# Performance work log

Measured on AMD Instinct MI355X. Metric: run time of the kernel, lower is better.

## Reference

```python
import jax, jax.numpy as jnp
import numpy as np

B, T, D = 2, 2048, 1024
H, DH = 16, 64          # num_heads, size_per_head
NU = H * DH             # num_units == 1024


def setup_inputs() -> dict:
    key = jax.random.key(0)
    ks = jax.random.split(key, 8)
    s = 0.02
    return {
        "queries": jax.random.normal(ks[0], (B, T, D), jnp.float32),
        "keys": jax.random.normal(ks[1], (B, T, D), jnp.float32),
        "Wq": jax.random.normal(ks[2], (D, NU), jnp.float32) * s,
        "bq": jnp.zeros((NU,), jnp.float32),
        "Wk": jax.random.normal(ks[3], (D, NU), jnp.float32) * s,
        "bk": jnp.zeros((NU,), jnp.float32),
        "Wv": jax.random.normal(ks[4], (D, NU), jnp.float32) * s,
        "bv": jnp.zeros((NU,), jnp.float32),
    }


def reference(queries, keys, Wq, bq, Wk, bk, Wv, bv):
    # QKV projections
    q = queries @ Wq + bq            # [B, T, NU]
    k = keys @ Wk + bk
    v = keys @ Wv + bv
    # split heads: [B, T, H, DH] -> [B, H, T, DH]
    q_ = q.reshape(B, T, H, DH).transpose(0, 2, 1, 3)
    k_ = k.reshape(B, T, H, DH).transpose(0, 2, 1, 3)
    v_ = v.reshape(B, T, H, DH).transpose(0, 2, 1, 3)
    # scores scaled by num_units**-0.5 (full hidden dim, as in source)
    scores = jnp.einsum("bhqd,bhkd->bhqk", q_, k_) * (NU ** -0.5)
    # causal mask: triu(ones).T == lower-triangular; zeros -> -inf
    causal = jnp.tril(jnp.ones((T, T), bool))
    scores = jnp.where(causal, scores, -jnp.inf)
    weights = jax.nn.softmax(scores, axis=-1)   # [B, H, T, T]
    # dropout is identity in eval/reference
    out = jnp.einsum("bhqk,bhkd->bhqd", weights, v_)  # [B, H, T, DH]
    # merge heads back to [B, T, NU]
    out = out.transpose(0, 2, 1, 3).reshape(B, T, NU)
    return out, weights
```

## Files before the change

kernel.cpp:

```cpp
#include <hip/hip_runtime.h>
#include <cstddef>
#include <cstdint>

namespace {
constexpr int B_ = 2, T_ = 2048, D_ = 1024, H_ = 16, DH_ = 64, NU_ = 1024;
constexpr float SCALE = 0.03125f;
constexpr size_t OUT_ELEMS = (size_t)B_ * T_ * NU_;
}

using f4  = __attribute__((ext_vector_type(4))) float;
using s8v = __attribute__((ext_vector_type(8))) short;
using s4v = __attribute__((ext_vector_type(4))) short;

#define MFMA16(a, b, c) __builtin_amdgcn_mfma_f32_16x16x32_bf16((a), (b), (c), 0, 0, 0)

__device__ __forceinline__ float4 ld4(const float* p) { return *reinterpret_cast<const float4*>(p); }
__device__ __forceinline__ void st4(float* p, const float4 v) { *reinterpret_cast<float4*>(p) = v; }
__device__ __forceinline__ short f2bf(float f) {
    union { float f; uint32_t u; } v{f};
    uint32_t r = (v.u + 0x7fffu + ((v.u >> 16) & 1u)) >> 16;
    return (short)r;
}

#if __has_builtin(__builtin_amdgcn_global_load_lds)
#define HAVE_GLOAD_LDS 1
__device__ __forceinline__ void load_lds16(const void* g, void* l) {
    __builtin_amdgcn_global_load_lds(
        (const __attribute__((address_space(1))) void*)g,
        (__attribute__((address_space(3))) void*)l, 16, 0, 0);
}
#else
#define HAVE_GLOAD_LDS 0
#endif

__global__ __launch_bounds__(256) void cvt_x_kernel(
    const float* __restrict__ q, const float* __restrict__ k,
    short* __restrict__ qx, short* __restrict__ kx)
{
    const float* src = blockIdx.y ? k : q;
    short* dst       = blockIdx.y ? kx : qx;
    size_t i = ((size_t)blockIdx.x * 256 + threadIdx.x) * 8;
    float4 a = ld4(src + i), b = ld4(src + i + 4);
    s8v o = { f2bf(a.x), f2bf(a.y), f2bf(a.z), f2bf(a.w),
              f2bf(b.x), f2bf(b.y), f2bf(b.z), f2bf(b.w) };
    *reinterpret_cast<s8v*>(dst + i) = o;
}

__global__ __launch_bounds__(256) void cvt_w_kernel(
    const float* __restrict__ Wq, const float* __restrict__ Wk,
    const float* __restrict__ Wv, short* __restrict__ wt3)
{
    const int z = blockIdx.z;
    const float* W = (z == 0) ? Wq : (z == 1) ? Wk : Wv;
    short* dst = wt3 + (size_t)z * D_ * NU_;
    const int n0 = blockIdx.x * 64, k0 = blockIdx.y * 64;
    __shared__ float tl[64][68];
    const int rr = threadIdx.x >> 2, cc = (threadIdx.x & 3) * 16;
    const float* s = W + (size_t)(k0 + rr) * NU_ + n0 + cc;
    st4(&tl[rr][cc + 0],  ld4(s + 0));
    st4(&tl[rr][cc + 4],  ld4(s + 4));
    st4(&tl[rr][cc + 8],  ld4(s + 8));
    st4(&tl[rr][cc + 12], ld4(s + 12));
    __syncthreads();
    short* d = dst + (size_t)(n0 + rr) * D_ + k0 + cc;
#pragma unroll
    for (int c = 0; c < 4; ++c) {
        s4v o = { f2bf(tl[cc + c * 4 + 0][rr]), f2bf(tl[cc + c * 4 + 1][rr]),
                  f2bf(tl[cc + c * 4 + 2][rr]), f2bf(tl[cc + c * 4 + 3][rr]) };
        *reinterpret_cast<s4v*>(d + c * 4) = o;
    }
}

__global__ __launch_bounds__(256) void proj_mfma(
    const short* __restrict__ qx, const short* __restrict__ kx,
    const short* __restrict__ wt3,
    const float* __restrict__ bq, const float* __restrict__ bk,
    const float* __restrict__ bv,
    short* __restrict__ qb, short* __restrict__ kb, short* __restrict__ vt)
{
    const int lin = blockIdx.z * 256 + blockIdx.y * 8 + blockIdx.x;
    const int virt = (lin & 7) * 96 + (lin >> 3);
    const int z = virt >> 8, rem = virt & 255;
    const int m0 = (rem >> 3) * 128, n0 = (rem & 7) * 128;

    const short* __restrict__ X  = (z == 0) ? qx : kx;
    const short* __restrict__ Wt = wt3 + (size_t)z * D_ * NU_;
    const float* __restrict__ bias = (z == 0) ? bq : (z == 1) ? bk : bv;

    const int t = threadIdx.x, w = t >> 6, l = t & 63;
    const int lr = l & 15, lg = l >> 4;
    const int wr = w >> 1, wc = w & 1;

    __shared__ short Asl[128 * 64];
    __shared__ short Bsl[128 * 64];

    f4 acc[4][4];
#pragma unroll
    for (int m = 0; m < 4; ++m)
#pragma unroll
        for (int n = 0; n < 4; ++n) acc[m][n] = (f4){0.f, 0.f, 0.f, 0.f};

    for (int k0 = 0; k0 < D_; k0 += 64) {
#if HAVE_GLOAD_LDS
#pragma unroll
        for (int j = 0; j < 4; ++j) {
            const int c0 = (w * 4 + j) * 64;
            const int c  = c0 + l;
            const int row = c >> 3, qo = (c & 7) * 8;
            load_lds16(X  + (size_t)(m0 + row) * D_ + k0 + qo, (char*)Asl + (size_t)c0 * 16);
            load_lds16(Wt + (size_t)(n0 + row) * D_ + k0 + qo, (char*)Bsl + (size_t)c0 * 16);
        }
        __syncthreads();
#else
        {
            const int sr = t >> 1, sc = (t & 1) * 32;
            s8v a0 = *reinterpret_cast<const s8v*>(X  + (size_t)(m0 + sr) * D_ + k0 + sc);
            s8v a1 = *reinterpret_cast<const s8v*>(X  + (size_t)(m0 + sr) * D_ + k0 + sc + 8);
            s8v a2 = *reinterpret_cast<const s8v*>(X  + (size_t)(m0 + sr) * D_ + k0 + sc + 16);
            s8v a3 = *reinterpret_cast<const s8v*>(X  + (size_t)(m0 + sr) * D_ + k0 + sc + 24);
            s8v b0 = *reinterpret_cast<const s8v*>(Wt + (size_t)(n0 + sr) * D_ + k0 + sc);
            s8v b1 = *reinterpret_cast<const s8v*>(Wt + (size_t)(n0 + sr) * D_ + k0 + sc + 8);
            s8v b2 = *reinterpret_cast<const s8v*>(Wt + (size_t)(n0 + sr) * D_ + k0 + sc + 16);
            s8v b3 = *reinterpret_cast<const s8v*>(Wt + (size_t)(n0 + sr) * D_ + k0 + sc + 24);
            __syncthreads();
            *reinterpret_cast<s8v*>(&Asl[sr * 64 + sc])      = a0;
            *reinterpret_cast<s8v*>(&Asl[sr * 64 + sc + 8])  = a1;
            *reinterpret_cast<s8v*>(&Asl[sr * 64 + sc + 16]) = a2;
            *reinterpret_cast<s8v*>(&Asl[sr * 64 + sc + 24]) = a3;
            *reinterpret_cast<s8v*>(&Bsl[sr * 64 + sc])      = b0;
            *reinterpret_cast<s8v*>(&Bsl[sr * 64 + sc + 8])  = b1;
            *reinterpret_cast<s8v*>(&Bsl[sr * 64 + sc + 16]) = b2;
            *reinterpret_cast<s8v*>(&Bsl[sr * 64 + sc + 24]) = b3;
            __syncthreads();
        }
#endif

#pragma unroll
        for (int kk = 0; kk < 2; ++kk) {
            s8v af[4], bf[4];
#pragma unroll
            for (int m = 0; m < 4; ++m)
                af[m] = *reinterpret_cast<const s8v*>(
                    &Asl[(wr * 64 + m * 16 + lr) * 64 + kk * 32 + lg * 8]);
#pragma unroll
            for (int n = 0; n < 4; ++n)
                bf[n] = *reinterpret_cast<const s8v*>(
                    &Bsl[(wc * 64 + n * 16 + lr) * 64 + kk * 32 + lg * 8]);
#pragma unroll
            for (int m = 0; m < 4; ++m)
#pragma unroll
                for (int n = 0; n < 4; ++n)
                    acc[m][n] = MFMA16(af[m], bf[n], acc[m][n]);
        }
        __syncthreads();
    }

    if (z < 2) {
        short* __restrict__ Y = (z == 0) ? qb : kb;
#pragma unroll
        for (int n = 0; n < 4; ++n) {
            const int col = n0 + wc * 64 + n * 16 + lr;
            const float bval = bias[col];
#pragma unroll
            for (int m = 0; m < 4; ++m) {
                const int row0 = m0 + wr * 64 + m * 16 + lg * 4;
#pragma unroll
                for (int r = 0; r < 4; ++r)
                    Y[(size_t)(row0 + r) * NU_ + col] = f2bf(acc[m][n][r] + bval);
            }
        }
    } else {
#pragma unroll
        for (int n = 0; n < 4; ++n) {
            const int col = n0 + wc * 64 + n * 16 + lr;
            const float bval = bias[col];
            const int hh = col >> 6, dd = col & 63;
#pragma unroll
            for (int m = 0; m < 4; ++m) {
                const int Mi = m0 + wr * 64 + m * 16 + lg * 4;
                const int bb = Mi >> 11, t0 = Mi & 2047;
                s4v o = { f2bf(acc[m][n][0] + bval), f2bf(acc[m][n][1] + bval),
                          f2bf(acc[m][n][2] + bval), f2bf(acc[m][n][3] + bval) };
                *reinterpret_cast<s4v*>(vt + ((size_t)(bb * 16 + hh) * 64 + dd) * T_ + t0) = o;
            }
        }
    }
}

__global__ __launch_bounds__(256) void attn_pv_mfma(
    const short* __restrict__ qb, const short* __restrict__ kb,
    const short* __restrict__ vt, float* __restrict__ rsws,
    float* __restrict__ out)
{
    const int lin = blockIdx.x;
    const int xcd = lin & 7, v = lin >> 3;
    const int bh  = xcd * 4 + (v >> 6);
    const int g32 = 63 - (v & 63);
    const int b = bh >> 4, h = bh & 15;
    const int r0 = g32 * 32;
    const int t = threadIdx.x, w = t >> 6, l = t & 63;
    const int lr = l & 15, lg = l >> 4;
    const int tile16 = (r0 + 31) >> 6;
    const int rlocA  = r0 - tile16 * 64 + lr;

    __shared__ __align__(16) char smem[16 * 1024 + 512];
    short* Pl    = (short*)smem;
    float* OA    = (float*)smem;
    float* rsbuf = (float*)(smem + 16 * 1024);

    const short* qrowA = qb + (size_t)(b * T_ + r0 + lr) * NU_ + h * DH_ + lg * 8;
    const s8v qA0 = *reinterpret_cast<const s8v*>(qrowA);
    const s8v qA1 = *reinterpret_cast<const s8v*>(qrowA + 32);
    const s8v qB0 = *reinterpret_cast<const s8v*>(qrowA + 16 * NU_);
    const s8v qB1 = *reinterpret_cast<const s8v*>(qrowA + 16 * NU_ + 32);

    f4 accA[4], accB[4];
#pragma unroll
    for (int nt = 0; nt < 4; ++nt) {
        accA[nt] = (f4){0.f, 0.f, 0.f, 0.f};
        accB[nt] = (f4){0.f, 0.f, 0.f, 0.f};
    }
    float rsumA = 0.f, rsumB = 0.f;
    const f4 zf = (f4){0.f, 0.f, 0.f, 0.f};
    const int sw = (lr & 7) << 3;
    const short* kbase0 = kb + (size_t)(b * T_) * NU_ + h * DH_ + lg * 8;
    short* const PlA = &Pl[w * 1024 + lr * 64];
    short* const PlB = &Pl[4096 + w * 1024 + lr * 64];

    for (int ch = w; ch <= tile16; ch += 4) {
        const int jc = ch * 64;
        const bool diag = (ch == tile16);
        const short* kbase = kbase0 + (size_t)jc * NU_;

#pragma unroll
        for (int nt = 0; nt < 4; ++nt) {
            const short* kr = kbase + (size_t)(nt * 16 + lr) * NU_;
            s8v kf0 = *reinterpret_cast<const s8v*>(kr);
            s8v kf1 = *reinterpret_cast<const s8v*>(kr + 32);
            f4 aA = MFMA16(kf0, qA0, zf);
            f4 sA = MFMA16(kf1, qA1, aA);
            f4 aB = MFMA16(kf0, qB0, zf);
            f4 sB = MFMA16(kf1, qB1, aB);

            const int jl = nt * 16 + lg * 4;
            float eA[4], eB[4];
#pragma unroll
            for (int r = 0; r < 4; ++r) {
                float vA = __expf(sA[r] * SCALE);
                float vB = __expf(sB[r] * SCALE);
                if (diag && (jl + r > rlocA))      vA = 0.f;
                if (diag && (jl + r > rlocA + 16)) vB = 0.f;
                eA[r] = vA; eB[r] = vB;
            }
            rsumA += (eA[0] + eA[1]) + (eA[2] + eA[3]);
            rsumB += (eB[0] + eB[1]) + (eB[2] + eB[3]);
            const int colp = jl ^ sw;
            s4v pA = { f2bf(eA[0]), f2bf(eA[1]), f2bf(eA[2]), f2bf(eA[3]) };
            s4v pB = { f2bf(eB[0]), f2bf(eB[1]), f2bf(eB[2]), f2bf(eB[3]) };
            *reinterpret_cast<s4v*>(PlA + colp) = pA;
            *reinterpret_cast<s4v*>(PlB + colp) = pB;
        }

        s8v pfA0 = *reinterpret_cast<const s8v*>(PlA + ((lg * 8) ^ sw));
        s8v pfA1 = *reinterpret_cast<const s8v*>(PlA + ((32 + lg * 8) ^ sw));
        s8v pfB0 = *reinterpret_cast<const s8v*>(PlB + ((lg * 8) ^ sw));
        s8v pfB1 = *reinterpret_cast<const s8v*>(PlB + ((32 + lg * 8) ^ sw));
#pragma unroll
        for (int nt = 0; nt < 4; ++nt) {
            const short* vr = vt + (size_t)(bh * 64 + nt * 16 + lr) * T_ + jc + lg * 8;
            s8v vf0 = *reinterpret_cast<const s8v*>(vr);
            s8v vf1 = *reinterpret_cast<const s8v*>(vr + 32);
            accA[nt] = MFMA16(pfA0, vf0, accA[nt]);
            accA[nt] = MFMA16(pfA1, vf1, accA[nt]);
            accB[nt] = MFMA16(pfB0, vf0, accB[nt]);
            accB[nt] = MFMA16(pfB1, vf1, accB[nt]);
        }
    }

    rsumA += __shfl_xor(rsumA, 16); rsumA += __shfl_xor(rsumA, 32);
    rsumB += __shfl_xor(rsumB, 16); rsumB += __shfl_xor(rsumB, 32);

    __syncthreads();
    if (lg == 0) {
        rsbuf[w * 16 + lr]      = rsumA;
        rsbuf[64 + w * 16 + lr] = rsumB;
    }

#pragma unroll
    for (int nt = 0; nt < 4; ++nt)
        st4(&OA[(size_t)(w * 64 + l) * 16 + nt * 4], *(const float4*)&accA[nt]);
    __syncthreads();
    {
        float osum[4] = {0.f, 0.f, 0.f, 0.f};
#pragma unroll
        for (int wv = 0; wv < 4; ++wv) {
            float4 p = *(const float4*)&OA[(size_t)(wv * 64 + l) * 16 + w * 4];
#pragma unroll
            for (int r = 0; r < 4; ++r) osum[r] += (&p.x)[r];
        }
#pragma unroll
        for (int r = 0; r < 4; ++r) {
            const int ro = lg * 4 + r;
            const float rt = rsbuf[ro] + rsbuf[16 + ro] + rsbuf[32 + ro] + rsbuf[48 + ro];
            out[(size_t)(b * T_ + r0 + ro) * NU_ + h * DH_ + w * 16 + lr] = osum[r] / rt;
        }
        if (w == 0 && t < 16) {
            rsws[(size_t)bh * T_ + r0 + t] =
                rsbuf[t] + rsbuf[16 + t] + rsbuf[32 + t] + rsbuf[48 + t];
            rsws[(size_t)bh * T_ + r0 + 16 + t] =
                rsbuf[64 + t] + rsbuf[80 + t] + rsbuf[96 + t] + rsbuf[112 + t];
        }
    }
    __syncthreads();

#pragma unroll
    for (int nt = 0; nt < 4; ++nt)
        st4(&OA[(size_t)(w * 64 + l) * 16 + nt * 4], *(const float4*)&accB[nt]);
    __syncthreads();
    {
        float osum[4] = {0.f, 0.f, 0.f, 0.f};
#pragma unroll
        for (int wv = 0; wv < 4; ++wv) {
            float4 p = *(const float4*)&OA[(size_t)(wv * 64 + l) * 16 + w * 4];
#pragma unroll
            for (int r = 0; r < 4; ++r) osum[r] += (&p.x)[r];
        }
#pragma unroll
        for (int r = 0; r < 4; ++r) {
            const int ro = lg * 4 + r;
            const float rt = rsbuf[64 + ro] + rsbuf[80 + ro] + rsbuf[96 + ro] + rsbuf[112 + ro];
            out[(size_t)(b * T_ + r0 + 16 + ro) * NU_ + h * DH_ + w * 16 + lr] = osum[r] / rt;
        }
    }
}

__global__ __launch_bounds__(256) void attn_wts_mfma(
    const short* __restrict__ qb, const short* __restrict__ kb,
    const float* __restrict__ rsws, float* __restrict__ wts)
{
    const int lin = blockIdx.x;
    const int xcd = lin & 7, v = lin >> 3;
    const int bh  = xcd * 4 + (v >> 7);
    const int rem = v & 127;
    const int qt2 = 15 - (rem >> 3);
    const int jb  = rem & 7;
    const int b = bh >> 4, h = bh & 15;
    const int r0 = qt2 * 128;
    const int chmax = 2 * qt2 + 1;
    const int t = threadIdx.x, w = t >> 6, l = t & 63;
    const int lr = l & 15, lg = l >> 4;

    const int iA = r0 + w * 16 + lr;
    const int iB = iA + 64;

    const short* qrowA = qb + (size_t)(b * T_ + iA) * NU_ + h * DH_ + lg * 8;
    const s8v qA0 = *reinterpret_cast<const s8v*>(qrowA);
    const s8v qA1 = *reinterpret_cast<const s8v*>(qrowA + 32);
    const s8v qB0 = *reinterpret_cast<const s8v*>(qrowA + 64 * NU_);
    const s8v qB1 = *reinterpret_cast<const s8v*>(qrowA + 64 * NU_ + 32);
    const f4 zf = (f4){0.f, 0.f, 0.f, 0.f};

    const float invA = 1.f / rsws[(size_t)bh * T_ + iA];
    const float invB = 1.f / rsws[(size_t)bh * T_ + iB];
    float* const wrowA = &wts[((size_t)bh * T_ + iA) * T_];
    float* const wrowB = &wts[((size_t)bh * T_ + iB) * T_];
    const short* kbase0 = kb + (size_t)(b * T_) * NU_ + h * DH_ + lg * 8;

#pragma unroll
    for (int cx = 0; cx < 4; ++cx) {
        const int ch = jb * 4 + cx;
        const int jc = ch * 64;
        if (ch <= chmax) {
            const short* kbase = kbase0 + (size_t)jc * NU_;
            f4 sA[4], sB[4];
#pragma unroll
            for (int nt = 0; nt < 4; ++nt) {
                const short* kr = kbase + (size_t)(nt * 16 + lr) * NU_;
                s8v kf0 = *reinterpret_cast<const s8v*>(kr);
                s8v kf1 = *reinterpret_cast<const s8v*>(kr + 32);
                f4 aA = MFMA16(kf0, qA0, zf);
                sA[nt] = MFMA16(kf1, qA1, aA);
                f4 aB = MFMA16(kf0, qB0, zf);
                sB[nt] = MFMA16(kf1, qB1, aB);
            }
#pragma unroll
            for (int nt = 0; nt < 4; ++nt) {
                float4 oA, oB;
                float* eA = &oA.x;
                float* eB = &oB.x;
#pragma unroll
                for (int r = 0; r < 4; ++r) {
                    const int j = jc + nt * 16 + lg * 4 + r;
                    eA[r] = (j <= iA) ? __expf(sA[nt][r] * SCALE) * invA : 0.f;
                    eB[r] = (j <= iB) ? __expf(sB[nt][r] * SCALE) * invB : 0.f;
                }
                st4(wrowA + jc + nt * 16 + lg * 4, oA);
                st4(wrowB + jc + nt * 16 + lg * 4, oB);
            }
        } else {
            const float4 z4 = make_float4(0.f, 0.f, 0.f, 0.f);
#pragma unroll
            for (int half = 0; half < 2; ++half) {
                float* dst = &wts[((size_t)bh * T_ + r0 + half * 64 + (t >> 2)) * T_
                                  + jc + (t & 3) * 16];
                st4(dst + 0, z4); st4(dst + 4, z4);
                st4(dst + 8, z4); st4(dst + 12, z4);
            }
        }
    }
}

extern "C" void kernel_launch(void* const* d_in, const int* in_sizes, int n_in,
                              void* d_out, int out_size, void* d_ws, size_t ws_size,
                              hipStream_t stream)
{
    const float* queries = (const float*)d_in[0];
    const float* keys    = (const float*)d_in[1];
    const float* Wq = (const float*)d_in[2];
    const float* bq = (const float*)d_in[3];
    const float* Wk = (const float*)d_in[4];
    const float* bk = (const float*)d_in[5];
    const float* Wv = (const float*)d_in[6];
    const float* bv = (const float*)d_in[7];

    float* out = (float*)d_out;
    float* wts = out + OUT_ELEMS;

    short* qx = (short*)d_ws;
    short* kx = qx + (size_t)B_ * T_ * D_;
    short* wt = kx + (size_t)B_ * T_ * D_;
    short* qb = wt + (size_t)3 * D_ * NU_;
    short* kb = qb + (size_t)B_ * T_ * NU_;
    short* vt = kb + (size_t)B_ * T_ * NU_;
    float* rsws = (float*)(vt + (size_t)B_ * T_ * NU_);

    cvt_x_kernel<<<dim3((B_ * T_ * D_) / 2048, 2), 256, 0, stream>>>(queries, keys, qx, kx);
    cvt_w_kernel<<<dim3(16, 16, 3), 256, 0, stream>>>(Wq, Wk, Wv, wt);
    proj_mfma<<<dim3(8, 32, 3), 256, 0, stream>>>(
        qx, kx, wt, bq, bk, bv, qb, kb, vt);
    attn_pv_mfma<<<dim3(2048), 256, 0, stream>>>(qb, kb, vt, rsws, out);
    attn_wts_mfma<<<dim3(4096), 256, 0, stream>>>(qb, kb, rsws, wts);
}
```

Baseline: 295.6 us.

## Process 64 query rows per block in attention PV kernel

The PV attention kernel now handles 64 query rows per block instead of 32, giving four 16-row sub-tiles per wave that share each K and V fragment load. Grid size drops from 2048 to 1024 blocks and shared memory for the P staging doubles. The aim is to halve redundant K/V global reads and the causal diagonal overhead. In exchange, register pressure rises (16 accumulators plus 8 Q fragments), occupancy may drop, and there are fewer blocks to balance the triangular workload.

```diff
diff --git a/kernel.cpp b/kernel.cpp
--- a/kernel.cpp
+++ b/kernel.cpp
@@ -194,38 +194,39 @@
 {
     const int lin = blockIdx.x;
     const int xcd = lin & 7, v = lin >> 3;
-    const int bh  = xcd * 4 + (v >> 6);
-    const int g32 = 63 - (v & 63);
+    const int bh  = xcd * 4 + (v >> 5);
+    const int g64 = 31 - (v & 31);
     const int b = bh >> 4, h = bh & 15;
-    const int r0 = g32 * 32;
+    const int r0 = g64 * 64;
     const int t = threadIdx.x, w = t >> 6, l = t & 63;
     const int lr = l & 15, lg = l >> 4;
-    const int tile16 = (r0 + 31) >> 6;
-    const int rlocA  = r0 - tile16 * 64 + lr;
-
-    __shared__ __align__(16) char smem[16 * 1024 + 512];
+    const int tile16 = g64;
+
+    __shared__ __align__(16) char smem[32 * 1024 + 1024];
     short* Pl    = (short*)smem;
     float* OA    = (float*)smem;
-    float* rsbuf = (float*)(smem + 16 * 1024);
-
-    const short* qrowA = qb + (size_t)(b * T_ + r0 + lr) * NU_ + h * DH_ + lg * 8;
-    const s8v qA0 = *reinterpret_cast<const s8v*>(qrowA);
-    const s8v qA1 = *reinterpret_cast<const s8v*>(qrowA + 32);
-    const s8v qB0 = *reinterpret_cast<const s8v*>(qrowA + 16 * NU_);
-    const s8v qB1 = *reinterpret_cast<const s8v*>(qrowA + 16 * NU_ + 32);
-
-    f4 accA[4], accB[4];
-#pragma unroll
-    for (int nt = 0; nt < 4; ++nt) {
-        accA[nt] = (f4){0.f, 0.f, 0.f, 0.f};
-        accB[nt] = (f4){0.f, 0.f, 0.f, 0.f};
-    }
-    float rsumA = 0.f, rsumB = 0.f;
+    float* rsbuf = (float*)(smem + 32 * 1024);
+
+    const short* qrow0 = qb + (size_t)(b * T_ + r0 + lr) * NU_ + h * DH_ + lg * 8;
+    s8v qf[4][2];
+#pragma unroll
+    for (int d = 0; d < 4; ++d) {
+        qf[d][0] = *reinterpret_cast<const s8v*>(qrow0 + (size_t)d * 16 * NU_);
+        qf[d][1] = *reinterpret_cast<const s8v*>(qrow0 + (size_t)d * 16 * NU_ + 32);
+    }
+
+    f4 acc[4][4];
+#pragma unroll
+    for (int d = 0; d < 4; ++d)
+#pragma unroll
+        for (int nt = 0; nt < 4; ++nt) acc[d][nt] = (f4){0.f, 0.f, 0.f, 0.f};
+    float rsum[4] = {0.f, 0.f, 0.f, 0.f};
     const f4 zf = (f4){0.f, 0.f, 0.f, 0.f};
     const int sw = (lr & 7) << 3;
     const short* kbase0 = kb + (size_t)(b * T_) * NU_ + h * DH_ + lg * 8;
-    short* const PlA = &Pl[w * 1024 + lr * 64];
-    short* const PlB = &Pl[4096 + w * 1024 + lr * 64];
+    short* PlW[4];
+#pragma unroll
+    for (int d = 0; d < 4; ++d) PlW[d] = &Pl[d * 4096 + w * 1024 + lr * 64];
 
     for (int ch = w; ch <= tile16; ch += 4) {
         const int jc = ch * 64;
@@ -237,60 +238,61 @@
             const short* kr = kbase + (size_t)(nt * 16 + lr) * NU_;
             s8v kf0 = *reinterpret_cast<const s8v*>(kr);
             s8v kf1 = *reinterpret_cast<const s8v*>(kr + 32);
-            f4 aA = MFMA16(kf0, qA0, zf);
-            f4 sA = MFMA16(kf1, qA1, aA);
-            f4 aB = MFMA16(kf0, qB0, zf);
-            f4 sB = MFMA16(kf1, qB1, aB);
-
             const int jl = nt * 16 + lg * 4;
-            float eA[4], eB[4];
-#pragma unroll
-            for (int r = 0; r < 4; ++r) {
-                float vA = __expf(sA[r] * SCALE);
-                float vB = __expf(sB[r] * SCALE);
-                if (diag && (jl + r > rlocA))      vA = 0.f;
-                if (diag && (jl + r > rlocA + 16)) vB = 0.f;
-                eA[r] = vA; eB[r] = vB;
-            }
-            rsumA += (eA[0] + eA[1]) + (eA[2] + eA[3]);
-            rsumB += (eB[0] + eB[1]) + (eB[2] + eB[3]);
-            const int colp = jl ^ sw;
-            s4v pA = { f2bf(eA[0]), f2bf(eA[1]), f2bf(eA[2]), f2bf(eA[3]) };
-            s4v pB = { f2bf(eB[0]), f2bf(eB[1]), f2bf(eB[2]), f2bf(eB[3]) };
-            *reinterpret_cast<s4v*>(PlA + colp) = pA;
-            *reinterpret_cast<s4v*>(PlB + colp) = pB;
-        }
-
-        s8v pfA0 = *reinterpret_cast<const s8v*>(PlA + ((lg * 8) ^ sw));
-        s8v pfA1 = *reinterpret_cast<const s8v*>(PlA + ((32 + lg * 8) ^ sw));
-        s8v pfB0 = *reinterpret_cast<const s8v*>(PlB + ((lg * 8) ^ sw));
-        s8v pfB1 = *reinterpret_cast<const s8v*>(PlB + ((32 + lg * 8) ^ sw));
+#pragma unroll
+            for (int d = 0; d < 4; ++d) {
+                f4 a = MFMA16(kf0, qf[d][0], zf);
+                f4 s = MFMA16(kf1, qf[d][1], a);
+                float e[4];
+#pragma unroll
+                for (int r = 0; r < 4; ++r) {
+                    float vv = __expf(s[r] * SCALE);
+                    if (diag && (jl + r > d * 16 + lr)) vv = 0.f;
+                    e[r] = vv;
+                }
+                rsum[d] += (e[0] + e[1]) + (e[2] + e[3]);
+                s4v pv = { f2bf(e[0]), f2bf(e[1]), f2bf(e[2]), f2bf(e[3]) };
+                *reinterpret_cast<s4v*>(PlW[d] + (jl ^ sw)) = pv;
+            }
+        }
+
+        s8v pf[4][2];
+#pragma unroll
+        for (int d = 0; d < 4; ++d) {
+            pf[d][0] = *reinterpret_cast<const s8v*>(PlW[d] + ((lg * 8) ^ sw));
+            pf[d][1] = *reinterpret_cast<const s8v*>(PlW[d] + ((32 + lg * 8) ^ sw));
+        }
 #pragma unroll
         for (int nt = 0; nt < 4; ++nt) {
             const short* vr = vt + (size_t)(bh * 64 + nt * 16 + lr) * T_ + jc + lg * 8;
             s8v vf0 = *reinterpret_cast<const s8v*>(vr);
             s8v vf1 = *reinterpret_cast<const s8v*>(vr + 32);
-            accA[nt] = MFMA16(pfA0, vf0, accA[nt]);
-            accA[nt] = MFMA16(pfA1, vf1, accA[nt]);
-            accB[nt] = MFMA16(pfB0, vf0, accB[nt]);
-            accB[nt] = MFMA16(pfB1, vf1, accB[nt]);
-        }
-    }
-
-    rsumA += __shfl_xor(rsumA, 16); rsumA += __shfl_xor(rsumA, 32);
-    rsumB += __shfl_xor(rsumB, 16); rsumB += __shfl_xor(rsumB, 32);
+#pragma unroll
+            for (int d = 0; d < 4; ++d) {
+                acc[d][nt] = MFMA16(pf[d][0], vf0, acc[d][nt]);
+                acc[d][nt] = MFMA16(pf[d][1], vf1, acc[d][nt]);
+            }
+        }
+    }
+
+#pragma unroll
+    for (int d = 0; d < 4; ++d) {
+        rsum[d] += __shfl_xor(rsum[d], 16);
+        rsum[d] += __shfl_xor(rsum[d], 32);
+    }
 
     __syncthreads();
     if (lg == 0) {
-        rsbuf[w * 16 + lr]      = rsumA;
-        rsbuf[64 + w * 16 + lr] = rsumB;
-    }
-
-#pragma unroll
-    for (int nt = 0; nt < 4; ++nt)
-        st4(&OA[(size_t)(w * 64 + l) * 16 + nt * 4], *(const float4*)&accA[nt]);
-    __syncthreads();
-    {
+#pragma unroll
+        for (int d = 0; d < 4; ++d) rsbuf[d * 64 + w * 16 + lr] = rsum[d];
+    }
+
+#pragma unroll
+    for (int d = 0; d < 4; ++d) {
+#pragma unroll
+        for (int nt = 0; nt < 4; ++nt)
+            st4(&OA[(size_t)(w * 64 + l) * 16 + nt * 4], *(const float4*)&acc[d][nt]);
+        __syncthreads();
         float osum[4] = {0.f, 0.f, 0.f, 0.f};
 #pragma unroll
         for (int wv = 0; wv < 4; ++wv) {
@@ -301,36 +303,16 @@
 #pragma unroll
         for (int r = 0; r < 4; ++r) {
             const int ro = lg * 4 + r;
-            const float rt = rsbuf[ro] + rsbuf[16 + ro] + rsbuf[32 + ro] + rsbuf[48 + ro];
-            out[(size_t)(b * T_ + r0 + ro) * NU_ + h * DH_ + w * 16 + lr] = osum[r] / rt;
-        }
-        if (w == 0 && t < 16) {
-            rsws[(size_t)bh * T_ + r0 + t] =
-                rsbuf[t] + rsbuf[16 + t] + rsbuf[32 + t] + rsbuf[48 + t];
-            rsws[(size_t)bh * T_ + r0 + 16 + t] =
-                rsbuf[64 + t] + rsbuf[80 + t] + rsbuf[96 + t] + rsbuf[112 + t];
-        }
-    }
-    __syncthreads();
-
-#pragma unroll
-    for (int nt = 0; nt < 4; ++nt)
-        st4(&OA[(size_t)(w * 64 + l) * 16 + nt * 4], *(const float4*)&accB[nt]);
-    __syncthreads();
-    {
-        float osum[4] = {0.f, 0.f, 0.f, 0.f};
-#pragma unroll
-        for (int wv = 0; wv < 4; ++wv) {
-            float4 p = *(const float4*)&OA[(size_t)(wv * 64 + l) * 16 + w * 4];
-#pragma unroll
-            for (int r = 0; r < 4; ++r) osum[r] += (&p.x)[r];
-        }
-#pragma unroll
-        for (int r = 0; r < 4; ++r) {
-            const int ro = lg * 4 + r;
-            const float rt = rsbuf[64 + ro] + rsbuf[80 + ro] + rsbuf[96 + ro] + rsbuf[112 + ro];
-            out[(size_t)(b * T_ + r0 + 16 + ro) * NU_ + h * DH_ + w * 16 + lr] = osum[r] / rt;
-        }
+            const float rt = rsbuf[d * 64 + ro] + rsbuf[d * 64 + 16 + ro]
+                           + rsbuf[d * 64 + 32 + ro] + rsbuf[d * 64 + 48 + ro];
+            out[(size_t)(b * T_ + r0 + d * 16 + ro) * NU_ + h * DH_ + w * 16 + lr] =
+                osum[r] / rt;
+        }
+        if (w == 0 && t < 16)
+            rsws[(size_t)bh * T_ + r0 + d * 16 + t] =
+                rsbuf[d * 64 + t] + rsbuf[d * 64 + 16 + t]
+                + rsbuf[d * 64 + 32 + t] + rsbuf[d * 64 + 48 + t];
+        __syncthreads();
     }
 }
 
@@ -438,6 +420,6 @@
     cvt_w_kernel<<<dim3(16, 16, 3), 256, 0, stream>>>(Wq, Wk, Wv, wt);
     proj_mfma<<<dim3(8, 32, 3), 256, 0, stream>>>(
         qx, kx, wt, bq, bk, bv, qb, kb, vt);
-    attn_pv_mfma<<<dim3(2048), 256, 0, stream>>>(qb, kb, vt, rsws, out);
+    attn_pv_mfma<<<dim3(1024), 256, 0, stream>>>(qb, kb, vt, rsws, out);
     attn_wts_mfma<<<dim3(4096), 256, 0, stream>>>(qb, kb, rsws, wts);
 }
```

Measured after the change: 283.8 us. 1.04x faster.
